# Performance work log

Hardware: AMD Instinct MI355X
Metric: run time of the kernel (lower is better)

The kernel has to match this reference:

```python
import jax, jax.numpy as jnp
import numpy as np

D_MODEL = 1024
H = 16
D_K = D_MODEL // H


def setup_inputs() -> dict:
    key = jax.random.key(0)
    ks = jax.random.split(key, 8)
    B, S = 2, 2048
    q = jax.random.normal(ks[0], (B, S, D_MODEL), dtype=jnp.float32)
    k = jax.random.normal(ks[1], (B, S, D_MODEL), dtype=jnp.float32)
    v = jax.random.normal(ks[2], (B, S, D_MODEL), dtype=jnp.float32)
    mask = jnp.ones((B, 1, S), dtype=jnp.int32)  # key-padding mask, 1 = keep
    sc = 1.0 / np.sqrt(D_MODEL)
    # torch Linear weights [out, in]
    Wq = jax.random.normal(ks[3], (D_MODEL, D_MODEL), dtype=jnp.float32) * sc
    Wk = jax.random.normal(ks[4], (D_MODEL, D_MODEL), dtype=jnp.float32) * sc
    Wv = jax.random.normal(ks[5], (D_MODEL, D_MODEL), dtype=jnp.float32) * sc
    Wo = jax.random.normal(ks[6], (D_MODEL, D_MODEL), dtype=jnp.float32) * sc
    return {"q": q, "k": k, "v": v, "mask": mask,
            "Wq": Wq, "Wk": Wk, "Wv": Wv, "Wo": Wo}


def reference(q, k, v, mask, Wq, Wk, Wv, Wo):
    B, Sq, _ = q.shape
    Sk = k.shape[1]
    # projections (torch Linear: x @ W.T), split heads -> [B, H, S, d_k]
    def split_heads(x, W, S):
        return (x @ W.T).reshape(B, S, H, D_K).transpose(0, 2, 1, 3)
    qh = split_heads(q, Wq, Sq)
    kh = split_heads(k, Wk, Sk)
    vh = split_heads(v, Wv, Sk)
    scores = jnp.einsum('bhqd,bhkd->bhqk', qh, kh) / jnp.sqrt(
        jnp.asarray(D_K, qh.dtype))
    # mask.unsqueeze(1): [B,1,S] -> [B,1,1,S]; masked_fill(mask==0, -1e9)
    m = mask[:, None, :, :]
    scores = jnp.where(m == 0, jnp.asarray(-1e9, scores.dtype), scores)
    p = jax.nn.softmax(scores, axis=-1)
    out = jnp.einsum('bhqk,bhkd->bhqd', p, vh)
    out = out.transpose(0, 2, 1, 3).reshape(B, Sq, H * D_K)
    return out @ Wo.T
```

## Files before the change

### kernel.cpp

```cpp
#include <hip/hip_runtime.h>
#include <hip/hip_bf16.h>

#define LOG2E 1.4426950408889634f

typedef __attribute__((ext_vector_type(8))) __bf16 bf16x8;
typedef __attribute__((ext_vector_type(2))) __bf16 bf16x2;
typedef __attribute__((ext_vector_type(4))) float f32x4;
typedef __attribute__((ext_vector_type(16))) float f32x16;
typedef __attribute__((ext_vector_type(2))) unsigned u32x2;

#define MFMA16(a,b,c) __builtin_amdgcn_mfma_f32_16x16x32_bf16((a),(b),(c),0,0,0)
#define MFMA32(a,b,c) __builtin_amdgcn_mfma_f32_32x32x16_bf16((a),(b),(c),0,0,0)

#define GLL16(g, l) __builtin_amdgcn_global_load_lds( \
    (const __attribute__((address_space(1))) void*)(g), \
    (__attribute__((address_space(3))) void*)(l), 16, 0, 0)

__device__ __forceinline__ unsigned short bfu(float f) {
    __bf16 h = (__bf16)f; unsigned short u; __builtin_memcpy(&u, &h, 2); return u;
}
__device__ __forceinline__ unsigned cvtpk(float lo, float hi) {
    bf16x2 t; t.x = (__bf16)lo; t.y = (__bf16)hi;
    unsigned r; __builtin_memcpy(&r, &t, 4); return r;
}
__device__ __forceinline__ bf16x8 cvt8(float4 a, float4 b, float s) {
    bf16x8 o;
    o[0]=(__bf16)(a.x*s); o[1]=(__bf16)(a.y*s); o[2]=(__bf16)(a.z*s); o[3]=(__bf16)(a.w*s);
    o[4]=(__bf16)(b.x*s); o[5]=(__bf16)(b.y*s); o[6]=(__bf16)(b.z*s); o[7]=(__bf16)(b.w*s);
    return o;
}

__global__ __launch_bounds__(256)
void conv_kernel(const float* __restrict__ q, const float* __restrict__ k,
                 const float* __restrict__ v, const float* __restrict__ Wq,
                 const float* __restrict__ Wk, const float* __restrict__ Wv,
                 const float* __restrict__ Wo, unsigned short* __restrict__ Xb,
                 unsigned short* __restrict__ Wb)
{
    const int y = blockIdx.y;
    if (y < 3) {
        const float* s = (y==0)?q:(y==1)?k:v;
        size_t i = ((size_t)blockIdx.x*256 + threadIdx.x)*8;
        float4 a = *(const float4*)(s+i), b = *(const float4*)(s+i+4);
        *(bf16x8*)(Xb + (size_t)y*4194304 + i) = cvt8(a, b, 1.0f);
    } else {
        const int w = blockIdx.x >> 9;
        const float* s = (w==0)?Wq:(w==1)?Wk:(w==2)?Wv:Wo;
        const float sc = (w==0) ? 0.125f*LOG2E : 1.0f;
        size_t i = ((size_t)(blockIdx.x & 511)*256 + threadIdx.x)*8;
        float4 a = *(const float4*)(s+i), b = *(const float4*)(s+i+4);
        *(bf16x8*)(Wb + (size_t)w*1048576 + i) = cvt8(a, b, sc);
    }
}

__global__ __launch_bounds__(256)
void qkv_kernel(const unsigned short* __restrict__ Xb,
                const unsigned short* __restrict__ Wb,
                unsigned short* __restrict__ Qh, unsigned short* __restrict__ Kh,
                unsigned short* __restrict__ Vt)
{
    __shared__ unsigned short As[2][4096];
    __shared__ unsigned short Bs[2][4096];
    const int z = blockIdx.z;
    const unsigned short* X = Xb + (size_t)z*4194304;
    const unsigned short* W = Wb + (size_t)z*1048576;
    const int t = threadIdx.x, wid = t>>6, lane = t&63;
    const int m0 = blockIdx.x*128, n0 = blockIdx.y*128;
    const int wr = (wid>>1)*64, wc = (wid&1)*64;
    const int lr = lane&15, lk = lane>>4;

    f32x4 acc[4][4] = {};

#pragma unroll
    for (int i=0;i<2;++i){
        int flat = i*4096 + wid*1024 + lane*16;
        int row = flat>>6, cb = (flat&63) ^ ((row&3)<<4);
        GLL16(X + (size_t)(m0+row)*1024 + (cb>>1), (char*)&As[0][0] + i*4096 + wid*1024);
        GLL16(W + (size_t)(n0+row)*1024 + (cb>>1), (char*)&Bs[0][0] + i*4096 + wid*1024);
    }
    asm volatile("s_waitcnt vmcnt(0)" ::: "memory");
    __builtin_amdgcn_s_barrier();
    asm volatile("" ::: "memory");

    for (int kt=0; kt<32; ++kt){
        const int cur = kt&1;
        if (kt<31){
            const int nb = cur^1, K0 = (kt+1)*32;
#pragma unroll
            for (int i=0;i<2;++i){
                int flat = i*4096 + wid*1024 + lane*16;
                int row = flat>>6, cb = (flat&63) ^ ((row&3)<<4);
                GLL16(X + (size_t)(m0+row)*1024 + K0 + (cb>>1), (char*)&As[nb][0] + i*4096 + wid*1024);
                GLL16(W + (size_t)(n0+row)*1024 + K0 + (cb>>1), (char*)&Bs[nb][0] + i*4096 + wid*1024);
            }
        }
        bf16x8 a[4], b[4];
#pragma unroll
        for (int i=0;i<4;++i){
            int row = wr+i*16+lr;
            a[i] = *(const bf16x8*)((const char*)&As[cur][0] + row*64 + ((lk*16)^((row&3)<<4)));
        }
#pragma unroll
        for (int j=0;j<4;++j){
            int row = wc+j*16+lr;
            b[j] = *(const bf16x8*)((const char*)&Bs[cur][0] + row*64 + ((lk*16)^((row&3)<<4)));
        }
#pragma unroll
        for (int i=0;i<4;++i)
#pragma unroll
            for (int j=0;j<4;++j)
                acc[i][j] = MFMA16(a[i], b[j], acc[i][j]);
        asm volatile("s_waitcnt vmcnt(0)" ::: "memory");
        __builtin_amdgcn_s_barrier();
        asm volatile("" ::: "memory");
    }

    unsigned short* out = (z==0)?Qh:(z==1)?Kh:Vt;
#pragma unroll
    for (int i=0;i<4;++i)
#pragma unroll
      for (int j=0;j<4;++j)
#pragma unroll
        for (int r=0;r<4;++r){
            int m = m0 + wr + i*16 + lk*4 + r;
            int n = n0 + wc + j*16 + lr;
            int b_ = m>>11, s = m&2047;
            int h = n>>6, d = n&63;
            size_t idx = (z==2) ? ((size_t)(b_*16+h)*64 + d)*2048 + s
                                : ((size_t)(b_*16+h)*2048 + s)*64 + d;
            out[idx] = bfu(acc[i][j][r]);
        }
}

__global__ __launch_bounds__(256)
void oproj_kernel(const unsigned short* __restrict__ Oh,
                  const unsigned short* __restrict__ Wo,
                  float* __restrict__ out)
{
    __shared__ unsigned short As[2][8192];
    __shared__ unsigned short Bs2[2][4096];
    const int t = threadIdx.x, wid = t>>6, lane = t&63;
    const int m0 = blockIdx.x*128, n0 = blockIdx.y*64;
    const int wr = (wid>>1)*64, wc = (wid&1)*32;
    const int lr = lane&15, lk = lane>>4;
    const int fbase = wid*1024 + lane*16;

    f32x4 acc[4][2] = {};

#pragma unroll
    for (int i=0;i<4;++i){
        int flat = i*4096 + fbase, row = flat>>7;
        int cb = (flat&127) ^ ((row&7)<<4);
        int m = m0+row, b_ = m>>11, s = m&2047;
        GLL16(Oh + ((size_t)(b_*16+0)*2048 + s)*64 + (cb>>1), (char*)&As[0][0] + i*4096 + wid*1024);
    }
#pragma unroll
    for (int i=0;i<2;++i){
        int flat = i*4096 + fbase, row = flat>>7;
        int cb = (flat&127) ^ ((row&7)<<4);
        GLL16(Wo + (size_t)(n0+row)*1024 + (cb>>1), (char*)&Bs2[0][0] + i*4096 + wid*1024);
    }

    for (int kt=0; kt<16; ++kt){
        const int cur = kt&1;
        if (kt<15){
            const int nb = cur^1, K0 = (kt+1)*64, h = K0>>6;
#pragma unroll
            for (int i=0;i<4;++i){
                int flat = i*4096 + fbase, row = flat>>7;
                int cb = (flat&127) ^ ((row&7)<<4);
                int m = m0+row, b_ = m>>11, s = m&2047;
                GLL16(Oh + ((size_t)(b_*16+h)*2048 + s)*64 + (cb>>1),
                      (char*)&As[nb][0] + i*4096 + wid*1024);
            }
#pragma unroll
            for (int i=0;i<2;++i){
                int flat = i*4096 + fbase, row = flat>>7;
                int cb = (flat&127) ^ ((row&7)<<4);
                GLL16(Wo + (size_t)(n0+row)*1024 + K0 + (cb>>1),
                      (char*)&Bs2[nb][0] + i*4096 + wid*1024);
            }
            asm volatile("s_waitcnt vmcnt(6)" ::: "memory");
        } else {
            asm volatile("s_waitcnt vmcnt(0)" ::: "memory");
        }
        __builtin_amdgcn_s_barrier();
        asm volatile("" ::: "memory");

        bf16x8 a[4][2], b[2][2];
#pragma unroll
        for (int i=0;i<4;++i){
            int row = wr+i*16+lr, sw = (row&7)<<4;
            const char* rp = (const char*)&As[cur][0] + row*128;
#pragma unroll
            for (int ks=0;ks<2;++ks)
                a[i][ks] = *(const bf16x8*)(rp + ((ks*64 + lk*16)^sw));
        }
#pragma unroll
        for (int j=0;j<2;++j){
            int row = wc+j*16+lr, sw = (row&7)<<4;
            const char* rp = (const char*)&Bs2[cur][0] + row*128;
#pragma unroll
            for (int ks=0;ks<2;++ks)
                b[j][ks] = *(const bf16x8*)(rp + ((ks*64 + lk*16)^sw));
        }
#pragma unroll
        for (int i=0;i<4;++i)
#pragma unroll
          for (int j=0;j<2;++j)
#pragma unroll
            for (int ks=0;ks<2;++ks)
                acc[i][j] = MFMA16(a[i][ks], b[j][ks], acc[i][j]);
        asm volatile("" ::: "memory");
        __builtin_amdgcn_s_barrier();
    }

#pragma unroll
    for (int i=0;i<4;++i)
#pragma unroll
      for (int j=0;j<2;++j)
#pragma unroll
        for (int r=0;r<4;++r){
            int m = m0 + wr + i*16 + lk*4 + r;
            int n = n0 + wc + j*16 + lr;
            out[(size_t)m*1024 + n] = acc[i][j][r];
        }
}

__global__ __launch_bounds__(128)
void attn_kernel(const unsigned short* __restrict__ Qh,
                 const unsigned short* __restrict__ Kh,
                 const unsigned short* __restrict__ Vt,
                 const int* __restrict__ mask,
                 unsigned short* __restrict__ Oh)
{
    __shared__ unsigned short Ks[2][4096];
    __shared__ unsigned short Vs[2][4096];
    __shared__ unsigned short Plds[2][2048];

    const int t = threadIdx.x, wid = t >> 6, lane = t & 63;
    const int l31 = lane & 31, hi = lane >> 5;
    const int linb = blockIdx.x + 32*blockIdx.y;
    const int work = (linb & 7)*128 + (linb >> 3);
    const int bh = work >> 5;
    const int q0 = (work & 31) * 64;
    const int b_ = bh >> 4;
    const int qw = q0 + wid*32 + l31;
    const int psw = (l31 & 7) << 4;

    unsigned flagbits;
    {
        const int4* mp = (const int4*)(mask + b_*2048 + (lane&31)*64);
        int bad = 0;
#pragma unroll
        for (int i=0;i<16;++i){ int4 m4 = mp[i];
            bad |= (m4.x==0)|(m4.y==0)|(m4.z==0)|(m4.w==0); }
        unsigned long long bm = __ballot(bad);
        flagbits = (unsigned)bm;
    }

    bf16x8 qf[4];
    const unsigned short* Qp = Qh + ((size_t)bh*2048 + qw)*64 + hi*8;
#pragma unroll
    for (int dc = 0; dc < 4; ++dc) qf[dc] = *(const bf16x8*)(Qp + dc*16);

    const unsigned short* Kbase = Kh + (size_t)bh*2048*64;
    const unsigned short* Vbase = Vt + (size_t)bh*64*2048;

#pragma unroll
    for (int c = 0; c < 4; ++c) {
        int row = c*16 + wid*8 + (lane>>3);
        int g = (lane&7) ^ (row&7);
        GLL16(Kbase + (size_t)row*64 + g*8,  &Ks[0][c*1024 + wid*512]);
        GLL16(Vbase + (size_t)row*2048 + g*8, &Vs[0][c*1024 + wid*512]);
    }

    f32x16 o0 = {}, o1 = {}, lacc = {};
    f32x16 minit;
#pragma unroll
    for (int r = 0; r < 16; ++r) minit[r] = -12.0f;

    bf16x8 ones;
    { union { unsigned u[4]; bf16x8 v; } tt;
      tt.u[0]=tt.u[1]=tt.u[2]=tt.u[3]=0x3F803F80u; ones = tt.v; }

    char* Pb = (char*)&Plds[wid][0];

    for (int kt = 0; kt < 32; ++kt) {
        const int cur = kt & 1;
        if (kt < 31) {
            const int nb = cur ^ 1;
#pragma unroll
            for (int c = 0; c < 4; ++c) {
                int row = c*16 + wid*8 + (lane>>3);
                int g = (lane&7) ^ (row&7);
                GLL16(Kbase + (size_t)((kt+1)*64 + row)*64 + g*8,  &Ks[nb][c*1024 + wid*512]);
                GLL16(Vbase + (size_t)row*2048 + (kt+1)*64 + g*8, &Vs[nb][c*1024 + wid*512]);
            }
            asm volatile("s_waitcnt vmcnt(8)" ::: "memory");
        } else {
            asm volatile("s_waitcnt vmcnt(0)" ::: "memory");
        }
        __builtin_amdgcn_s_barrier();
        asm volatile("" ::: "memory");

        const unsigned short* KsB = Ks[cur];
        const unsigned short* VsB = Vs[cur];

        f32x16 s0, s1;
        {
            const unsigned short* kr0 = KsB + (size_t)l31*64;
            const unsigned short* kr1 = KsB + (size_t)(32 + l31)*64;
#pragma unroll
            for (int dc = 0; dc < 4; ++dc) {
                int off = (dc*16 + hi*8) ^ (psw >> 1);
                bf16x8 k0 = *(const bf16x8*)(kr0 + off);
                bf16x8 k1 = *(const bf16x8*)(kr1 + off);
                if (dc == 0) { s0 = MFMA32(k0, qf[0], minit); s1 = MFMA32(k1, qf[0], minit); }
                else         { s0 = MFMA32(k0, qf[dc], s0);   s1 = MFMA32(k1, qf[dc], s1); }
            }
        }

        if (flagbits & (1u << kt)) {
            const int* mrow = mask + b_*2048 + kt*64;
#pragma unroll
            for (int r = 0; r < 16; ++r) {
                int kv = (r&3) + 8*(r>>2) + 4*hi;
                if (mrow[kv] == 0)      s0[r] = -1e9f;
                if (mrow[32 + kv] == 0) s1[r] = -1e9f;
            }
        }

#pragma unroll
        for (int r = 0; r < 16; ++r) {
            s0[r] = __builtin_amdgcn_exp2f(s0[r]);
            s1[r] = __builtin_amdgcn_exp2f(s1[r]);
        }

#pragma unroll
        for (int g = 0; g < 4; ++g) {
            int kvb = 16*g + 8*hi;
            u32x2 w0 = { cvtpk(s0[4*g],s0[4*g+1]), cvtpk(s0[4*g+2],s0[4*g+3]) };
            u32x2 w1 = { cvtpk(s1[4*g],s1[4*g+1]), cvtpk(s1[4*g+2],s1[4*g+3]) };
            *(u32x2*)(Pb + l31*128 + (kvb ^ psw))      = w0;
            *(u32x2*)(Pb + l31*128 + ((kvb+64) ^ psw)) = w1;
        }
        asm volatile("s_waitcnt lgkmcnt(0)" ::: "memory");
        bf16x8 pa[4];
#pragma unroll
        for (int kc = 0; kc < 4; ++kc)
            pa[kc] = *(const bf16x8*)(Pb + l31*128 + ((kc*32 + hi*16) ^ psw));

        {
            const unsigned short* vr0 = VsB + (size_t)l31*64;
            const unsigned short* vr1 = VsB + (size_t)(32 + l31)*64;
#pragma unroll
            for (int kc = 0; kc < 4; ++kc) {
                int off = (kc*16 + hi*8) ^ (psw >> 1);
                bf16x8 v0 = *(const bf16x8*)(vr0 + off);
                bf16x8 v1 = *(const bf16x8*)(vr1 + off);
                o0 = MFMA32(pa[kc], v0, o0);
                o1 = MFMA32(pa[kc], v1, o1);
                lacc = MFMA32(pa[kc], ones, lacc);
            }
        }
        asm volatile("" ::: "memory");
        __builtin_amdgcn_s_barrier();
    }

    unsigned short* Ob = Oh + ((size_t)bh*2048 + q0 + wid*32)*64;
#pragma unroll
    for (int r = 0; r < 16; ++r) {
        int qr = (r&3) + 8*(r>>2) + 4*hi;
        float inv = 1.0f / lacc[r];
        Ob[(size_t)qr*64 + l31]      = bfu(o0[r] * inv);
        Ob[(size_t)qr*64 + 32 + l31] = bfu(o1[r] * inv);
    }
}

extern "C" void kernel_launch(void* const* d_in, const int* in_sizes, int n_in,
                              void* d_out, int out_size, void* d_ws, size_t ws_size,
                              hipStream_t stream)
{
    const float* q  = (const float*)d_in[0];
    const float* k  = (const float*)d_in[1];
    const float* v  = (const float*)d_in[2];
    const int* mask = (const int*)d_in[3];
    const float* Wq = (const float*)d_in[4];
    const float* Wk = (const float*)d_in[5];
    const float* Wv = (const float*)d_in[6];
    const float* Wo = (const float*)d_in[7];
    float* out = (float*)d_out;

    unsigned short* Xb = (unsigned short*)d_ws;
    unsigned short* Wb = Xb + (size_t)12582912;
    unsigned short* Qh = Wb + (size_t)4194304;
    unsigned short* Kh = Qh + (size_t)4194304;
    unsigned short* Vt = Kh + (size_t)4194304;
    unsigned short* Oh = Xb;

    conv_kernel<<<dim3(2048,4), 256, 0, stream>>>(q, k, v, Wq, Wk, Wv, Wo, Xb, Wb);
    qkv_kernel<<<dim3(32,8,3), 256, 0, stream>>>(Xb, Wb, Qh, Kh, Vt);
    attn_kernel<<<dim3(32,32), 128, 0, stream>>>(Qh, Kh, Vt, mask, Oh);
    oproj_kernel<<<dim3(32,16), 256, 0, stream>>>(Oh, Wb + (size_t)3145728, out);
}
```

Before: 141.6 us.

## Keep softmax probabilities in registers and widen attention blocks to four waves

The attention kernel no longer writes P through LDS. It packs the exp'd score accumulators straight into bf16 MFMA A-operands and compensates by reading V with a permuted 8-byte-pair pattern matching the accumulator row order. Blocks grow to 256 threads covering 128 queries, so each K/V tile loaded into LDS is shared by four waves instead of two. This halves global K/V traffic per query and removes an LDS round trip and wait per tile, at the cost of more register pressure and narrower 8-byte LDS reads for V.

```diff
diff --git a/kernel.cpp b/kernel.cpp
--- a/kernel.cpp
+++ b/kernel.cpp
@@ -7,7 +7,6 @@
 typedef __attribute__((ext_vector_type(2))) __bf16 bf16x2;
 typedef __attribute__((ext_vector_type(4))) float f32x4;
 typedef __attribute__((ext_vector_type(16))) float f32x16;
-typedef __attribute__((ext_vector_type(2))) unsigned u32x2;
 
 #define MFMA16(a,b,c) __builtin_amdgcn_mfma_f32_16x16x32_bf16((a),(b),(c),0,0,0)
 #define MFMA32(a,b,c) __builtin_amdgcn_mfma_f32_32x32x16_bf16((a),(b),(c),0,0,0)
@@ -22,6 +21,9 @@
 __device__ __forceinline__ unsigned cvtpk(float lo, float hi) {
     bf16x2 t; t.x = (__bf16)lo; t.y = (__bf16)hi;
     unsigned r; __builtin_memcpy(&r, &t, 4); return r;
+}
+__device__ __forceinline__ bf16x8 pack4(unsigned a, unsigned b, unsigned c, unsigned d) {
+    union { unsigned u[4]; bf16x8 v; } t; t.u[0]=a; t.u[1]=b; t.u[2]=c; t.u[3]=d; return t.v;
 }
 __device__ __forceinline__ bf16x8 cvt8(float4 a, float4 b, float s) {
     bf16x8 o;
@@ -227,7 +229,7 @@
         }
 }
 
-__global__ __launch_bounds__(128)
+__global__ __launch_bounds__(256)
 void attn_kernel(const unsigned short* __restrict__ Qh,
                  const unsigned short* __restrict__ Kh,
                  const unsigned short* __restrict__ Vt,
@@ -236,17 +238,15 @@
 {
     __shared__ unsigned short Ks[2][4096];
     __shared__ unsigned short Vs[2][4096];
-    __shared__ unsigned short Plds[2][2048];
 
     const int t = threadIdx.x, wid = t >> 6, lane = t & 63;
     const int l31 = lane & 31, hi = lane >> 5;
-    const int linb = blockIdx.x + 32*blockIdx.y;
-    const int work = (linb & 7)*128 + (linb >> 3);
-    const int bh = work >> 5;
-    const int q0 = (work & 31) * 64;
+    const int linb = blockIdx.x + 16*blockIdx.y;
+    const int work = (linb & 7)*64 + (linb >> 3);
+    const int bh = work >> 4;
+    const int q0 = (work & 15) * 128;
     const int b_ = bh >> 4;
     const int qw = q0 + wid*32 + l31;
-    const int psw = (l31 & 7) << 4;
 
     unsigned flagbits;
     {
@@ -268,11 +268,11 @@
     const unsigned short* Vbase = Vt + (size_t)bh*64*2048;
 
 #pragma unroll
-    for (int c = 0; c < 4; ++c) {
-        int row = c*16 + wid*8 + (lane>>3);
+    for (int i = 0; i < 2; ++i) {
+        int row = wid*16 + i*8 + (lane>>3);
         int g = (lane&7) ^ (row&7);
-        GLL16(Kbase + (size_t)row*64 + g*8,  &Ks[0][c*1024 + wid*512]);
-        GLL16(Vbase + (size_t)row*2048 + g*8, &Vs[0][c*1024 + wid*512]);
+        GLL16(Kbase + (size_t)row*64 + g*8,  (char*)&Ks[0][0] + (wid*16+i*8)*128);
+        GLL16(Vbase + (size_t)row*2048 + g*8, (char*)&Vs[0][0] + (wid*16+i*8)*128);
     }
 
     f32x16 o0 = {}, o1 = {}, lacc = {};
@@ -284,20 +284,20 @@
     { union { unsigned u[4]; bf16x8 v; } tt;
       tt.u[0]=tt.u[1]=tt.u[2]=tt.u[3]=0x3F803F80u; ones = tt.v; }
 
-    char* Pb = (char*)&Plds[wid][0];
+    const int swz = (l31 & 7) << 3;
 
     for (int kt = 0; kt < 32; ++kt) {
         const int cur = kt & 1;
         if (kt < 31) {
             const int nb = cur ^ 1;
 #pragma unroll
-            for (int c = 0; c < 4; ++c) {
-                int row = c*16 + wid*8 + (lane>>3);
+            for (int i = 0; i < 2; ++i) {
+                int row = wid*16 + i*8 + (lane>>3);
                 int g = (lane&7) ^ (row&7);
-                GLL16(Kbase + (size_t)((kt+1)*64 + row)*64 + g*8,  &Ks[nb][c*1024 + wid*512]);
-                GLL16(Vbase + (size_t)row*2048 + (kt+1)*64 + g*8, &Vs[nb][c*1024 + wid*512]);
-            }
-            asm volatile("s_waitcnt vmcnt(8)" ::: "memory");
+                GLL16(Kbase + (size_t)((kt+1)*64 + row)*64 + g*8,  (char*)&Ks[nb][0] + (wid*16+i*8)*128);
+                GLL16(Vbase + (size_t)row*2048 + (kt+1)*64 + g*8, (char*)&Vs[nb][0] + (wid*16+i*8)*128);
+            }
+            asm volatile("s_waitcnt vmcnt(4)" ::: "memory");
         } else {
             asm volatile("s_waitcnt vmcnt(0)" ::: "memory");
         }
@@ -313,7 +313,7 @@
             const unsigned short* kr1 = KsB + (size_t)(32 + l31)*64;
 #pragma unroll
             for (int dc = 0; dc < 4; ++dc) {
-                int off = (dc*16 + hi*8) ^ (psw >> 1);
+                int off = (dc*16 + hi*8) ^ swz;
                 bf16x8 k0 = *(const bf16x8*)(kr0 + off);
                 bf16x8 k1 = *(const bf16x8*)(kr1 + off);
                 if (dc == 0) { s0 = MFMA32(k0, qf[0], minit); s1 = MFMA32(k1, qf[0], minit); }
@@ -321,6 +321,23 @@
             }
         }
 
+        bf16x8 vf0[4], vf1[4];
+        {
+            const unsigned short* vr0 = VsB + (size_t)l31*64;
+            const unsigned short* vr1 = VsB + (size_t)(32 + l31)*64;
+#pragma unroll
+            for (int kc = 0; kc < 4; ++kc) {
+                union { unsigned long long q2[2]; bf16x8 v; } a, b;
+                int o0u = (kc*16 + 4*hi) ^ swz;
+                int o1u = (kc*16 + 8 + 4*hi) ^ swz;
+                a.q2[0] = *(const unsigned long long*)(vr0 + o0u);
+                a.q2[1] = *(const unsigned long long*)(vr0 + o1u);
+                b.q2[0] = *(const unsigned long long*)(vr1 + o0u);
+                b.q2[1] = *(const unsigned long long*)(vr1 + o1u);
+                vf0[kc] = a.v; vf1[kc] = b.v;
+            }
+        }
+
         if (flagbits & (1u << kt)) {
             const int* mrow = mask + b_*2048 + kt*64;
 #pragma unroll
@@ -337,32 +354,21 @@
             s1[r] = __builtin_amdgcn_exp2f(s1[r]);
         }
 
-#pragma unroll
-        for (int g = 0; g < 4; ++g) {
-            int kvb = 16*g + 8*hi;
-            u32x2 w0 = { cvtpk(s0[4*g],s0[4*g+1]), cvtpk(s0[4*g+2],s0[4*g+3]) };
-            u32x2 w1 = { cvtpk(s1[4*g],s1[4*g+1]), cvtpk(s1[4*g+2],s1[4*g+3]) };
-            *(u32x2*)(Pb + l31*128 + (kvb ^ psw))      = w0;
-            *(u32x2*)(Pb + l31*128 + ((kvb+64) ^ psw)) = w1;
-        }
-        asm volatile("s_waitcnt lgkmcnt(0)" ::: "memory");
         bf16x8 pa[4];
-#pragma unroll
-        for (int kc = 0; kc < 4; ++kc)
-            pa[kc] = *(const bf16x8*)(Pb + l31*128 + ((kc*32 + hi*16) ^ psw));
-
-        {
-            const unsigned short* vr0 = VsB + (size_t)l31*64;
-            const unsigned short* vr1 = VsB + (size_t)(32 + l31)*64;
-#pragma unroll
-            for (int kc = 0; kc < 4; ++kc) {
-                int off = (kc*16 + hi*8) ^ (psw >> 1);
-                bf16x8 v0 = *(const bf16x8*)(vr0 + off);
-                bf16x8 v1 = *(const bf16x8*)(vr1 + off);
-                o0 = MFMA32(pa[kc], v0, o0);
-                o1 = MFMA32(pa[kc], v1, o1);
-                lacc = MFMA32(pa[kc], ones, lacc);
-            }
+        pa[0] = pack4(cvtpk(s0[0],s0[1]),  cvtpk(s0[2],s0[3]),
+                      cvtpk(s0[4],s0[5]),  cvtpk(s0[6],s0[7]));
+        pa[1] = pack4(cvtpk(s0[8],s0[9]),  cvtpk(s0[10],s0[11]),
+                      cvtpk(s0[12],s0[13]),cvtpk(s0[14],s0[15]));
+        pa[2] = pack4(cvtpk(s1[0],s1[1]),  cvtpk(s1[2],s1[3]),
+                      cvtpk(s1[4],s1[5]),  cvtpk(s1[6],s1[7]));
+        pa[3] = pack4(cvtpk(s1[8],s1[9]),  cvtpk(s1[10],s1[11]),
+                      cvtpk(s1[12],s1[13]),cvtpk(s1[14],s1[15]));
+
+#pragma unroll
+        for (int kc = 0; kc < 4; ++kc) {
+            o0 = MFMA32(pa[kc], vf0[kc], o0);
+            o1 = MFMA32(pa[kc], vf1[kc], o1);
+            lacc = MFMA32(pa[kc], ones, lacc);
         }
         asm volatile("" ::: "memory");
         __builtin_amdgcn_s_barrier();
@@ -401,6 +407,6 @@
 
     conv_kernel<<<dim3(2048,4), 256, 0, stream>>>(q, k, v, Wq, Wk, Wv, Wo, Xb, Wb);
     qkv_kernel<<<dim3(32,8,3), 256, 0, stream>>>(Xb, Wb, Qh, Kh, Vt);
-    attn_kernel<<<dim3(32,32), 128, 0, stream>>>(Qh, Kh, Vt, mask, Oh);
+    attn_kernel<<<dim3(16,32), 256, 0, stream>>>(Qh, Kh, Vt, mask, Oh);
     oproj_kernel<<<dim3(32,16), 256, 0, stream>>>(Oh, Wb + (size_t)3145728, out);
 }
```

Result: faster. 136.9 us (-3.3%).
